# Optimization experiments

Hardware: AMD Instinct MI355X
Metric: run time of the kernel (lower is better)

Reference implementation:

```python
import jax, jax.numpy as jnp
import numpy as np
import math

B, L, D = 4, 1024, 1024
N_HEAD, D_K, D_V = 16, 64, 64
LN_EPS = 1e-5


def setup_inputs() -> dict:
    key = jax.random.key(0)
    ks = jax.random.split(key, 10)
    q = jax.random.normal(ks[0], (B, L, D), dtype=jnp.float32)
    k = jax.random.normal(ks[1], (B, L, D), dtype=jnp.float32)
    v = jax.random.normal(ks[2], (B, L, D), dtype=jnp.float32)
    seq_len = jax.random.randint(ks[3], (B,), 1, L + 1, dtype=jnp.int32)
    std_qk = math.sqrt(2.0 / (D + D_K))
    std_v = math.sqrt(2.0 / (D + D_V))
    w_qs = jax.random.normal(ks[4], (N_HEAD * D_K, D), dtype=jnp.float32) * std_qk
    w_ks = jax.random.normal(ks[5], (N_HEAD * D_K, D), dtype=jnp.float32) * std_qk
    w_vs = jax.random.normal(ks[6], (N_HEAD * D_V, D), dtype=jnp.float32) * std_v
    b_qs = jnp.zeros((N_HEAD * D_K,), jnp.float32)
    b_ks = jnp.zeros((N_HEAD * D_K,), jnp.float32)
    b_vs = jnp.zeros((N_HEAD * D_V,), jnp.float32)
    std_fc = math.sqrt(2.0 / (N_HEAD * D_V + D))  # xavier normal
    fc_w = jax.random.normal(ks[7], (D, N_HEAD * D_V), dtype=jnp.float32) * std_fc
    fc_b = jnp.zeros((D,), jnp.float32)
    ln_g = jnp.ones((D,), jnp.float32)
    ln_b = jnp.zeros((D,), jnp.float32)
    return {"q": q, "k": k, "v": v, "seq_len": seq_len,
            "w_qs": w_qs, "b_qs": b_qs, "w_ks": w_ks, "b_ks": b_ks,
            "w_vs": w_vs, "b_vs": b_vs, "fc_w": fc_w, "fc_b": fc_b,
            "ln_g": ln_g, "ln_b": ln_b}


def reference(q, k, v, seq_len, w_qs, b_qs, w_ks, b_ks, w_vs, b_vs, fc_w, fc_b, ln_g, ln_b):
    sz_b, len_q, _ = q.shape
    len_k = k.shape[1]
    residual = q
    # projections -> [B, H, L, d]
    qh = (q @ w_qs.T + b_qs).reshape(sz_b, len_q, N_HEAD, D_K).transpose(0, 2, 1, 3)
    kh = (k @ w_ks.T + b_ks).reshape(sz_b, len_k, N_HEAD, D_K).transpose(0, 2, 1, 3)
    vh = (v @ w_vs.T + b_vs).reshape(sz_b, len_k, N_HEAD, D_V).transpose(0, 2, 1, 3)
    temperature = math.sqrt(D_K)
    attn = jnp.einsum('bhqd,bhkd->bhqk', qh, kh) / temperature  # [B,H,Lq,Lk]
    idx_k = jnp.arange(len_k)
    key_mask = idx_k[None, None, :] >= seq_len[:, None, None]   # [B,1,Lk]
    attn = jnp.where(key_mask[:, None, :, :], -jnp.inf, attn)
    attn = jax.nn.softmax(attn, axis=-1)
    idx_q = jnp.arange(len_q)
    query_mask = idx_q[None, :, None] >= seq_len[:, None, None]  # [B,Lq,1]
    attn = jnp.where(query_mask[:, None, :, :], 0.0, attn)
    # dropout is identity in eval mode
    out = jnp.einsum('bhqk,bhkd->bhqd', attn, vh)  # [B,H,Lq,Dv]
    out = out.transpose(0, 2, 1, 3).reshape(sz_b, len_q, N_HEAD * D_V)
    out = out @ fc_w.T + fc_b
    x = out + residual
    mu = jnp.mean(x, axis=-1, keepdims=True)
    var = jnp.mean((x - mu) ** 2, axis=-1, keepdims=True)
    output = (x - mu) * jax.lax.rsqrt(var + LN_EPS) * ln_g + ln_b
    # match torch layout: (n_head*sz_b, len_q, len_k)
    attn_ret = attn.transpose(1, 0, 2, 3).reshape(N_HEAD * sz_b, len_q, len_k)
    return (output, attn_ret)
```

## Files before the change

kernel.cpp:

```cpp
#include <hip/hip_runtime.h>
#include <math.h>

#define NB 4
#define SL 1024
#define DM 1024
#define NH 16
#define HD 64

typedef short v8s __attribute__((ext_vector_type(8)));
typedef float v4f __attribute__((ext_vector_type(4)));
typedef float v8f __attribute__((ext_vector_type(8)));
typedef unsigned short u16;
typedef unsigned int u32;

__device__ __forceinline__ v4f mfma_bf16(v8s a, v8s b, v4f c) {
  return __builtin_amdgcn_mfma_f32_16x16x32_bf16(a, b, c, 0, 0, 0);
}
__device__ __forceinline__ float bf2f(u16 x) {
  union { unsigned int u; float f; } cv; cv.u = ((unsigned int)x) << 16; return cv.f;
}
__device__ __forceinline__ u16 f2bf(float f) {
  union { float f; unsigned int u; } cv; cv.f = f;
  unsigned int r = cv.u + 0x7FFFu + ((cv.u >> 16) & 1u);
  return (u16)(r >> 16);
}
__device__ __forceinline__ v8s cvt8h(const float* p) {
  v8f x = *reinterpret_cast<const v8f*>(p);
  v8s h;
#pragma unroll
  for (int j = 0; j < 8; ++j) h[j] = (short)f2bf(x[j]);
  return h;
}
__device__ __forceinline__ void gl16(const u16* g, u16* lds_base_uniform) {
  __builtin_amdgcn_global_load_lds(
      (const __attribute__((address_space(1))) u32*)g,
      (__attribute__((address_space(3))) u32*)lds_base_uniform, 16, 0, 0);
}

__global__ __launch_bounds__(256) void cvt_qkv(
    const float* __restrict__ q, const float* __restrict__ k,
    const float* __restrict__ v, u16* __restrict__ qxb,
    u16* __restrict__ kxb, u16* __restrict__ vxb) {
  const unsigned total = 3u << 20;
  for (unsigned g = blockIdx.x * 256 + threadIdx.x; g < total;
       g += gridDim.x * 256) {
    unsigned r = g >> 20, local = g & ((1u << 20) - 1), i = local * 4;
    const float* src = (r == 0) ? q : (r == 1) ? k : v;
    u16* dst = (r == 0) ? qxb : (r == 1) ? kxb : vxb;
    float4 x = *reinterpret_cast<const float4*>(src + i);
    ushort4 h;
    h.x = f2bf(x.x); h.y = f2bf(x.y); h.z = f2bf(x.z); h.w = f2bf(x.w);
    *reinterpret_cast<ushort4*>(dst + i) = h;
  }
}
__global__ __launch_bounds__(256) void cvt_w4(
    const float* __restrict__ wq, const float* __restrict__ wk,
    const float* __restrict__ wv, const float* __restrict__ fw,
    u16* __restrict__ wqb, u16* __restrict__ wkb, u16* __restrict__ wvb,
    u16* __restrict__ fwb) {
  const unsigned total = 4u << 18;
  for (unsigned g = blockIdx.x * 256 + threadIdx.x; g < total;
       g += gridDim.x * 256) {
    unsigned r = g >> 18, local = g & ((1u << 18) - 1), i = local * 4;
    const float* src = (r == 0) ? wq : (r == 1) ? wk : (r == 2) ? wv : fw;
    u16* dst = (r == 0) ? wqb : (r == 1) ? wkb : (r == 2) ? wvb : fwb;
    float4 x = *reinterpret_cast<const float4*>(src + i);
    ushort4 h;
    h.x = f2bf(x.x); h.y = f2bf(x.y); h.z = f2bf(x.z); h.w = f2bf(x.w);
    *reinterpret_cast<ushort4*>(dst + i) = h;
  }
}

__global__ __launch_bounds__(256) void gemm_proj(
    const u16* __restrict__ qxb, const u16* __restrict__ kxb,
    const u16* __restrict__ vxb, const u16* __restrict__ wqb,
    const u16* __restrict__ wkb, const u16* __restrict__ wvb,
    const float* __restrict__ b_qs, const float* __restrict__ b_ks,
    const float* __restrict__ b_vs, const int* __restrict__ seq_len,
    u16* __restrict__ qh, u16* __restrict__ kh, u16* __restrict__ vt) {
  __shared__ u16 As[128 * 32];
  __shared__ u16 Bs[128 * 32];
  const int bid = blockIdx.x;
  const int sel = bid >> 8;
  const int tb = bid & 255;
  const int row0 = (tb >> 3) * 128;
  const int col0 = (tb & 7) * 128;
  const int bb = row0 >> 10, pos0 = row0 & (SL - 1);
  const bool dead = pos0 >= seq_len[bb];

  const int tid = threadIdx.x;
  const int wid = tid >> 6, l = tid & 63, lo4 = l & 15, hi2 = l >> 4;
  const int wm = wid >> 1, wn = wid & 1;

  v4f acc[4][4];
#pragma unroll
  for (int i = 0; i < 4; ++i)
#pragma unroll
    for (int j = 0; j < 4; ++j) acc[i][j] = (v4f){0.f, 0.f, 0.f, 0.f};

  if (!dead) {
    const u16* Xb = (sel == 0) ? qxb : (sel == 1) ? kxb : vxb;
    const u16* Wb = (sel == 0) ? wqb : (sel == 1) ? wkb : wvb;
    const int r0s = tid >> 2, c0s = (tid & 3) * 8;
    const int r1s = (tid + 256) >> 2;
    const int ub0 = (wid * 64) * 8;
    const int ub1 = (256 + wid * 64) * 8;
    for (int ks = 0; ks < 32; ++ks) {
      const int k0 = ks * 32;
      gl16(Xb + (size_t)(row0 + r0s) * DM + k0 + c0s, As + ub0);
      gl16(Xb + (size_t)(row0 + r1s) * DM + k0 + c0s, As + ub1);
      gl16(Wb + (size_t)(col0 + r0s) * DM + k0 + c0s, Bs + ub0);
      gl16(Wb + (size_t)(col0 + r1s) * DM + k0 + c0s, Bs + ub1);
      __syncthreads();
      v8s af[4], bf[4];
#pragma unroll
      for (int mi = 0; mi < 4; ++mi)
        af[mi] = *(const v8s*)&As[(wm * 64 + mi * 16 + lo4) * 32 + hi2 * 8];
#pragma unroll
      for (int ni = 0; ni < 4; ++ni)
        bf[ni] = *(const v8s*)&Bs[(wn * 64 + ni * 16 + lo4) * 32 + hi2 * 8];
#pragma unroll
      for (int mi = 0; mi < 4; ++mi)
#pragma unroll
        for (int ni = 0; ni < 4; ++ni)
          acc[mi][ni] = mfma_bf16(af[mi], bf[ni], acc[mi][ni]);
      __syncthreads();
    }
  }

  const float* bias = (sel == 0) ? b_qs : (sel == 1) ? b_ks : b_vs;
#pragma unroll
  for (int mi = 0; mi < 4; ++mi)
#pragma unroll
    for (int ni = 0; ni < 4; ++ni)
#pragma unroll
      for (int r = 0; r < 4; ++r) {
        int row = row0 + wm * 64 + mi * 16 + hi2 * 4 + r;
        int col = col0 + wn * 64 + ni * 16 + lo4;
        u16 ob = dead ? (u16)0 : f2bf(acc[mi][ni][r] + bias[col]);
        int b_ = row >> 10, pos = row & (SL - 1);
        int h = col >> 6, d = col & (HD - 1);
        if (sel < 2) {
          u16* out = sel ? kh : qh;
          out[((size_t)(b_ * NH + h) * SL + pos) * HD + d] = ob;
        } else {
          vt[((size_t)(b_ * NH + h) * HD + d) * SL + pos] = ob;
        }
      }
}

__global__ __launch_bounds__(256) void attn_kernel(
    const u16* __restrict__ qh, const u16* __restrict__ kh,
    const u16* __restrict__ vt, const int* __restrict__ seq_len,
    float* __restrict__ attn_out, float* __restrict__ ctx) {
  const int bh = blockIdx.x;
  const int qt = blockIdx.y;
  const int b_ = bh >> 4, h = bh & 15;
  const int seqb = seq_len[b_];
  const int tid = threadIdx.x;

  float* aout = attn_out + ((size_t)(h * NB + b_) * SL + qt * 16) * SL;

  if (qt * 16 >= seqb) {
    const float4 z = make_float4(0.f, 0.f, 0.f, 0.f);
#pragma unroll
    for (int i = 0; i < 16; ++i) {
      int idx = (tid + i * 256) * 4;
      int row = idx >> 10, key = idx & 1023;
      *reinterpret_cast<float4*>(&aout[(size_t)row * SL + key]) = z;
    }
    int r2 = tid >> 4, c2 = (tid & 15) * 4;
    *reinterpret_cast<float4*>(
        &ctx[((size_t)b_ * SL + qt * 16 + r2) * DM + h * HD + c2]) = z;
    return;
  }

  const int wv = tid >> 6, l = tid & 63;
  const int lo4 = l & 15, hi2 = l >> 4;

  __shared__ u16 p_lds[16][1032];
  __shared__ float red_m[4][16];
  __shared__ float red_s[4][16];

  const u16* qp = qh + ((size_t)bh * SL + qt * 16 + lo4) * HD + hi2 * 8;
  v8s aq0 = *(const v8s*)(qp);
  v8s aq1 = *(const v8s*)(qp + 32);

  const int kbase = wv * 256;
  const u16* Kb = kh + (size_t)bh * SL * HD;

  v4f s[16];
#pragma unroll
  for (int kt = 0; kt < 16; ++kt) {
    const bool kact = (kbase + kt * 16) < seqb;
    v4f acc = (v4f){0.f, 0.f, 0.f, 0.f};
    int key = kbase + kt * 16 + lo4;
    if (kact) {
      const u16* kp = Kb + key * HD + hi2 * 8;
      v8s bk0 = *(const v8s*)kp;
      v8s bk1 = *(const v8s*)(kp + 32);
      acc = mfma_bf16(aq0, bk0, acc);
      acc = mfma_bf16(aq1, bk1, acc);
    }
    bool km = key >= seqb;
#pragma unroll
    for (int r = 0; r < 4; ++r)
      s[kt][r] = km ? -INFINITY : acc[r] * 0.125f;
  }

  float m[4];
#pragma unroll
  for (int r = 0; r < 4; ++r) {
    float mm = s[0][r];
#pragma unroll
    for (int kt = 1; kt < 16; ++kt) mm = fmaxf(mm, s[kt][r]);
    for (int d2 = 1; d2 < 16; d2 <<= 1) mm = fmaxf(mm, __shfl_xor(mm, d2));
    m[r] = mm;
  }
  if (lo4 == 0) {
#pragma unroll
    for (int r = 0; r < 4; ++r) red_m[wv][hi2 * 4 + r] = m[r];
  }
  __syncthreads();
#pragma unroll
  for (int r = 0; r < 4; ++r) {
    float mm = red_m[0][hi2 * 4 + r];
    mm = fmaxf(mm, red_m[1][hi2 * 4 + r]);
    mm = fmaxf(mm, red_m[2][hi2 * 4 + r]);
    mm = fmaxf(mm, red_m[3][hi2 * 4 + r]);
    m[r] = mm;
  }
  float sm[4] = {0.f, 0.f, 0.f, 0.f};
#pragma unroll
  for (int kt = 0; kt < 16; ++kt) {
#pragma unroll
    for (int r = 0; r < 4; ++r) {
      float p = __expf(s[kt][r] - m[r]);
      s[kt][r] = p;
      sm[r] += p;
    }
  }
#pragma unroll
  for (int r = 0; r < 4; ++r)
    for (int d2 = 1; d2 < 16; d2 <<= 1) sm[r] += __shfl_xor(sm[r], d2);
  if (lo4 == 0) {
#pragma unroll
    for (int r = 0; r < 4; ++r) red_s[wv][hi2 * 4 + r] = sm[r];
  }
  __syncthreads();
  float inv[4];
#pragma unroll
  for (int r = 0; r < 4; ++r) {
    float t = red_s[0][hi2 * 4 + r] + red_s[1][hi2 * 4 + r] +
              red_s[2][hi2 * 4 + r] + red_s[3][hi2 * 4 + r];
    inv[r] = 1.f / t;
  }
#pragma unroll
  for (int r = 0; r < 4; ++r) {
    int row = hi2 * 4 + r;
    bool qm = (qt * 16 + row) >= seqb;
    float sc = qm ? 0.f : inv[r];
#pragma unroll
    for (int kt = 0; kt < 16; ++kt) {
      int key = kbase + kt * 16 + lo4;
      p_lds[row][key] = f2bf(s[kt][r] * sc);
    }
  }
  __syncthreads();
#pragma unroll
  for (int i = 0; i < 16; ++i) {
    int idx = (tid + i * 256) * 4;
    int row = idx >> 10, key = idx & 1023;
    ushort4 pv = *(const ushort4*)&p_lds[row][key];
    float4 o4 = make_float4(bf2f(pv.x), bf2f(pv.y), bf2f(pv.z), bf2f(pv.w));
    *reinterpret_cast<float4*>(&aout[(size_t)row * SL + key]) = o4;
  }
  v4f o = (v4f){0.f, 0.f, 0.f, 0.f};
  const u16* vbase = vt + (size_t)bh * HD * SL + (wv * 16 + lo4) * SL + hi2 * 8;
#pragma unroll 8
  for (int c = 0; c < 32; ++c) {
    if (c * 32 < seqb) {
      v8s pa = *(const v8s*)&p_lds[lo4][c * 32 + hi2 * 8];
      v8s vb = *(const v8s*)(vbase + c * 32);
      o = mfma_bf16(pa, vb, o);
    }
  }
#pragma unroll
  for (int r = 0; r < 4; ++r) {
    int row = qt * 16 + hi2 * 4 + r;
    ctx[((size_t)b_ * SL + row) * DM + h * HD + wv * 16 + lo4] = o[r];
  }
}

__global__ __launch_bounds__(256) void gemm_fc(
    const float* __restrict__ ctx, const u16* __restrict__ fcwb,
    const float* __restrict__ fcb, const float* __restrict__ resid,
    const int* __restrict__ seq_len, float* __restrict__ fcout) {
  __shared__ u16 As[128 * 32];
  __shared__ u16 Bs[128 * 32];
  const int row0 = (blockIdx.x >> 3) * 128;
  const int col0 = (blockIdx.x & 7) * 128;
  const int bb = row0 >> 10, pos0 = row0 & (SL - 1);
  const bool dead = pos0 >= seq_len[bb];
  const int tid = threadIdx.x;
  const int wid = tid >> 6, l = tid & 63, lo4 = l & 15, hi2 = l >> 4;
  const int wm = wid >> 1, wn = wid & 1;

  v4f acc[4][4];
#pragma unroll
  for (int i = 0; i < 4; ++i)
#pragma unroll
    for (int j = 0; j < 4; ++j) acc[i][j] = (v4f){0.f, 0.f, 0.f, 0.f};

  if (!dead) {
    const int r0s = tid >> 2, c0s = (tid & 3) * 8;
    const int r1s = (tid + 256) >> 2;
    const int ub0 = (wid * 64) * 8;
    const int ub1 = (256 + wid * 64) * 8;
    for (int ks = 0; ks < 32; ++ks) {
      const int k0 = ks * 32;
      gl16(fcwb + (size_t)(col0 + r0s) * DM + k0 + c0s, Bs + ub0);
      gl16(fcwb + (size_t)(col0 + r1s) * DM + k0 + c0s, Bs + ub1);
      *(v8s*)&As[tid * 8] = cvt8h(ctx + (size_t)(row0 + r0s) * DM + k0 + c0s);
      *(v8s*)&As[(tid + 256) * 8] =
          cvt8h(ctx + (size_t)(row0 + r1s) * DM + k0 + c0s);
      __syncthreads();
      v8s af[4], bf[4];
#pragma unroll
      for (int mi = 0; mi < 4; ++mi)
        af[mi] = *(const v8s*)&As[(wm * 64 + mi * 16 + lo4) * 32 + hi2 * 8];
#pragma unroll
      for (int ni = 0; ni < 4; ++ni)
        bf[ni] = *(const v8s*)&Bs[(wn * 64 + ni * 16 + lo4) * 32 + hi2 * 8];
#pragma unroll
      for (int mi = 0; mi < 4; ++mi)
#pragma unroll
        for (int ni = 0; ni < 4; ++ni)
          acc[mi][ni] = mfma_bf16(af[mi], bf[ni], acc[mi][ni]);
      __syncthreads();
    }
  }
#pragma unroll
  for (int mi = 0; mi < 4; ++mi)
#pragma unroll
    for (int ni = 0; ni < 4; ++ni)
#pragma unroll
      for (int r = 0; r < 4; ++r) {
        int row = row0 + wm * 64 + mi * 16 + hi2 * 4 + r;
        int col = col0 + wn * 64 + ni * 16 + lo4;
        fcout[(size_t)row * DM + col] =
            acc[mi][ni][r] + fcb[col] + resid[(size_t)row * DM + col];
      }
}

__global__ __launch_bounds__(256) void ln_rows(
    const float* __restrict__ x, const float* __restrict__ lng,
    const float* __restrict__ lnb, float* __restrict__ out) {
  const int row = blockIdx.x * 4 + (threadIdx.x >> 6);
  const int l = threadIdx.x & 63;
  const float* xr = x + (size_t)row * DM;
  float4 v[4];
  float s = 0.f, q2 = 0.f;
#pragma unroll
  for (int j = 0; j < 4; ++j) {
    v[j] = *reinterpret_cast<const float4*>(xr + l * 4 + j * 256);
    s += v[j].x + v[j].y + v[j].z + v[j].w;
    q2 += v[j].x * v[j].x + v[j].y * v[j].y + v[j].z * v[j].z + v[j].w * v[j].w;
  }
#pragma unroll
  for (int d = 1; d < 64; d <<= 1) {
    s += __shfl_xor(s, d);
    q2 += __shfl_xor(q2, d);
  }
  const float mean = s * (1.f / DM);
  const float var = q2 * (1.f / DM) - mean * mean;
  const float rstd = rsqrtf(var + 1e-5f);
#pragma unroll
  for (int j = 0; j < 4; ++j) {
    int c = l * 4 + j * 256;
    float4 g = *reinterpret_cast<const float4*>(lng + c);
    float4 b = *reinterpret_cast<const float4*>(lnb + c);
    float4 y;
    y.x = (v[j].x - mean) * rstd * g.x + b.x;
    y.y = (v[j].y - mean) * rstd * g.y + b.y;
    y.z = (v[j].z - mean) * rstd * g.z + b.z;
    y.w = (v[j].w - mean) * rstd * g.w + b.w;
    *reinterpret_cast<float4*>(out + (size_t)row * DM + c) = y;
  }
}

extern "C" void kernel_launch(void* const* d_in, const int* in_sizes, int n_in,
                              void* d_out, int out_size, void* d_ws, size_t ws_size,
                              hipStream_t stream) {
  const float* q = (const float*)d_in[0];
  const float* k = (const float*)d_in[1];
  const float* v = (const float*)d_in[2];
  const int* seq_len = (const int*)d_in[3];
  const float* w_qs = (const float*)d_in[4];
  const float* b_qs = (const float*)d_in[5];
  const float* w_ks = (const float*)d_in[6];
  const float* b_ks = (const float*)d_in[7];
  const float* w_vs = (const float*)d_in[8];
  const float* b_vs = (const float*)d_in[9];
  const float* fcw = (const float*)d_in[10];
  const float* fcb = (const float*)d_in[11];
  const float* lng = (const float*)d_in[12];
  const float* lnb = (const float*)d_in[13];

  float* out0 = (float*)d_out;
  float* attn_out = out0 + (size_t)NB * SL * DM;

  const size_t PLANE = (size_t)NB * SL * DM;
  const size_t WSZ = (size_t)DM * DM;
  u16* wsu = (u16*)d_ws;
  u16* qh = wsu;
  u16* kh = wsu + PLANE;
  u16* vt = wsu + 2 * PLANE;
  u16* fcwb = wsu + 3 * PLANE;
  float* ctx = out0;

  u16* satt = (u16*)attn_out;
  u16* qxb = satt;
  u16* kxb = satt + PLANE;
  u16* vxb = satt + 2 * PLANE;
  u16* wqb = satt + 3 * PLANE;
  u16* wkb = satt + 3 * PLANE + WSZ;
  u16* wvb = satt + 3 * PLANE + 2 * WSZ;

  float* fcout = (float*)d_ws;

  cvt_qkv<<<3072, 256, 0, stream>>>(q, k, v, qxb, kxb, vxb);
  cvt_w4<<<1024, 256, 0, stream>>>(w_qs, w_ks, w_vs, fcw, wqb, wkb, wvb, fcwb);
  gemm_proj<<<768, 256, 0, stream>>>(qxb, kxb, vxb, wqb, wkb, wvb,
                                     b_qs, b_ks, b_vs, seq_len, qh, kh, vt);
  attn_kernel<<<dim3(64, 64), 256, 0, stream>>>(qh, kh, vt, seq_len, attn_out, ctx);
  gemm_fc<<<256, 256, 0, stream>>>(ctx, fcwb, fcb, q, seq_len, fcout);
  ln_rows<<<1024, 256, 0, stream>>>(fcout, lng, lnb, out0);
}
```

Baseline: 170.4 us.

## Fuse activation bf16 conversion into projection GEMM and swap attention grid axes

After: 182.4 us. 1.07x slower.

```diff
diff --git a/kernel.cpp b/kernel.cpp
--- a/kernel.cpp
+++ b/kernel.cpp
@@ -37,22 +37,6 @@
       (__attribute__((address_space(3))) u32*)lds_base_uniform, 16, 0, 0);
 }
 
-__global__ __launch_bounds__(256) void cvt_qkv(
-    const float* __restrict__ q, const float* __restrict__ k,
-    const float* __restrict__ v, u16* __restrict__ qxb,
-    u16* __restrict__ kxb, u16* __restrict__ vxb) {
-  const unsigned total = 3u << 20;
-  for (unsigned g = blockIdx.x * 256 + threadIdx.x; g < total;
-       g += gridDim.x * 256) {
-    unsigned r = g >> 20, local = g & ((1u << 20) - 1), i = local * 4;
-    const float* src = (r == 0) ? q : (r == 1) ? k : v;
-    u16* dst = (r == 0) ? qxb : (r == 1) ? kxb : vxb;
-    float4 x = *reinterpret_cast<const float4*>(src + i);
-    ushort4 h;
-    h.x = f2bf(x.x); h.y = f2bf(x.y); h.z = f2bf(x.z); h.w = f2bf(x.w);
-    *reinterpret_cast<ushort4*>(dst + i) = h;
-  }
-}
 __global__ __launch_bounds__(256) void cvt_w4(
     const float* __restrict__ wq, const float* __restrict__ wk,
     const float* __restrict__ wv, const float* __restrict__ fw,
@@ -72,8 +56,8 @@
 }
 
 __global__ __launch_bounds__(256) void gemm_proj(
-    const u16* __restrict__ qxb, const u16* __restrict__ kxb,
-    const u16* __restrict__ vxb, const u16* __restrict__ wqb,
+    const float* __restrict__ qf, const float* __restrict__ kf,
+    const float* __restrict__ vf, const u16* __restrict__ wqb,
     const u16* __restrict__ wkb, const u16* __restrict__ wvb,
     const float* __restrict__ b_qs, const float* __restrict__ b_ks,
     const float* __restrict__ b_vs, const int* __restrict__ seq_len,
@@ -99,7 +83,7 @@
     for (int j = 0; j < 4; ++j) acc[i][j] = (v4f){0.f, 0.f, 0.f, 0.f};
 
   if (!dead) {
-    const u16* Xb = (sel == 0) ? qxb : (sel == 1) ? kxb : vxb;
+    const float* Xf = (sel == 0) ? qf : (sel == 1) ? kf : vf;
     const u16* Wb = (sel == 0) ? wqb : (sel == 1) ? wkb : wvb;
     const int r0s = tid >> 2, c0s = (tid & 3) * 8;
     const int r1s = (tid + 256) >> 2;
@@ -107,10 +91,11 @@
     const int ub1 = (256 + wid * 64) * 8;
     for (int ks = 0; ks < 32; ++ks) {
       const int k0 = ks * 32;
-      gl16(Xb + (size_t)(row0 + r0s) * DM + k0 + c0s, As + ub0);
-      gl16(Xb + (size_t)(row0 + r1s) * DM + k0 + c0s, As + ub1);
       gl16(Wb + (size_t)(col0 + r0s) * DM + k0 + c0s, Bs + ub0);
       gl16(Wb + (size_t)(col0 + r1s) * DM + k0 + c0s, Bs + ub1);
+      *(v8s*)&As[tid * 8] = cvt8h(Xf + (size_t)(row0 + r0s) * DM + k0 + c0s);
+      *(v8s*)&As[(tid + 256) * 8] =
+          cvt8h(Xf + (size_t)(row0 + r1s) * DM + k0 + c0s);
       __syncthreads();
       v8s af[4], bf[4];
 #pragma unroll
@@ -153,8 +138,8 @@
     const u16* __restrict__ qh, const u16* __restrict__ kh,
     const u16* __restrict__ vt, const int* __restrict__ seq_len,
     float* __restrict__ attn_out, float* __restrict__ ctx) {
-  const int bh = blockIdx.x;
-  const int qt = blockIdx.y;
+  const int qt = blockIdx.x;
+  const int bh = blockIdx.y;
   const int b_ = bh >> 4, h = bh & 15;
   const int seqb = seq_len[b_];
   const int tid = threadIdx.x;
@@ -420,18 +405,14 @@
   float* ctx = out0;
 
   u16* satt = (u16*)attn_out;
-  u16* qxb = satt;
-  u16* kxb = satt + PLANE;
-  u16* vxb = satt + 2 * PLANE;
-  u16* wqb = satt + 3 * PLANE;
-  u16* wkb = satt + 3 * PLANE + WSZ;
-  u16* wvb = satt + 3 * PLANE + 2 * WSZ;
+  u16* wqb = satt;
+  u16* wkb = satt + WSZ;
+  u16* wvb = satt + 2 * WSZ;
 
   float* fcout = (float*)d_ws;
 
-  cvt_qkv<<<3072, 256, 0, stream>>>(q, k, v, qxb, kxb, vxb);
   cvt_w4<<<1024, 256, 0, stream>>>(w_qs, w_ks, w_vs, fcw, wqb, wkb, wvb, fcwb);
-  gemm_proj<<<768, 256, 0, stream>>>(qxb, kxb, vxb, wqb, wkb, wvb,
+  gemm_proj<<<768, 256, 0, stream>>>(q, k, v, wqb, wkb, wvb,
                                      b_qs, b_ks, b_vs, seq_len, qh, kh, vt);
   attn_kernel<<<dim3(64, 64), 256, 0, stream>>>(qh, kh, vt, seq_len, attn_out, ctx);
   gemm_fc<<<256, 256, 0, stream>>>(ctx, fcwb, fcb, q, seq_len, fcout);
```
